# Kernel optimization log

Measured on AMD Instinct MI355X. Metric: run time of the kernel, lower is better.

## Reference

```python
import jax, jax.numpy as jnp
import numpy as np

D_MODEL = 2048
N_HEADS = 16
D_HEAD = 128
N_GROUPS = 4          # KV heads = N_HEADS // N_GROUPS = 4
D_FF = 2048           # hard-coded default in FeedForward
EPS = 1e-6


def setup_inputs() -> dict:
    key = jax.random.key(0)
    ks = jax.random.split(key, 16)
    B, S = 4, 1024
    Hkv = N_HEADS // N_GROUPS
    s = 0.02
    inp = {
        "x": jax.random.normal(ks[0], (B, S, D_MODEL), jnp.float32),
        "scale1": jnp.ones((D_MODEL,), jnp.float32),
        "Wq": jax.random.normal(ks[1], (D_MODEL, N_HEADS * D_HEAD), jnp.float32) * s,
        "bq": jnp.zeros((N_HEADS * D_HEAD,), jnp.float32),
        "Wk": jax.random.normal(ks[2], (D_MODEL, Hkv * D_HEAD), jnp.float32) * s,
        "bk": jnp.zeros((Hkv * D_HEAD,), jnp.float32),
        "Wv": jax.random.normal(ks[3], (D_MODEL, Hkv * D_HEAD), jnp.float32) * s,
        "bv": jnp.zeros((Hkv * D_HEAD,), jnp.float32),
        "Wo": jax.random.normal(ks[4], (N_HEADS * D_HEAD, D_MODEL), jnp.float32) * s,
        "bo": jnp.zeros((D_MODEL,), jnp.float32),
        "W1": jax.random.normal(ks[5], (D_MODEL, D_FF), jnp.float32) * s,
        "b1": jnp.zeros((D_FF,), jnp.float32),
        "W2": jax.random.normal(ks[6], (D_FF, D_MODEL), jnp.float32) * s,
        "b2": jnp.zeros((D_MODEL,), jnp.float32),
    }
    return inp


def _rmsnorm(x, scale):
    rms = jnp.sqrt(jnp.mean(x * x, axis=-1, keepdims=True) + EPS)
    return scale * (x / rms)


def reference(x, scale1, Wq, bq, Wk, bk, Wv, bv, Wo, bo, W1, b1, W2, b2):
    B, S, _ = x.shape
    Hkv = N_HEADS // N_GROUPS
    xn = _rmsnorm(x, scale1)  # [B,S,D]

    # GQA attention (prefill, step=None -> no cache)
    Q = (xn @ Wq + bq).reshape(B, S, N_HEADS, D_HEAD).transpose(0, 2, 1, 3)  # [B,H,S,d]
    K = (xn @ Wk + bk).reshape(B, S, Hkv, D_HEAD).transpose(0, 2, 1, 3)      # [B,Hkv,S,d]
    V = (xn @ Wv + bv).reshape(B, S, Hkv, D_HEAD).transpose(0, 2, 1, 3)
    Kr = jnp.repeat(K, N_GROUPS, axis=1)  # [B,H,S,d]
    Vr = jnp.repeat(V, N_GROUPS, axis=1)
    scores = jnp.einsum("bhqd,bhkd->bhqk", Q, Kr) / jnp.sqrt(jnp.float32(D_HEAD))
    attn = jax.nn.softmax(scores, axis=-1)
    out = jnp.einsum("bhqk,bhkd->bhqd", attn, Vr)  # [B,H,S,d]
    out = out.transpose(0, 2, 1, 3).reshape(B, S, N_HEADS * D_HEAD)
    x = x + out @ Wo + bo

    # Source bug preserved: FFN consumes rms_norm1 output, rms_norm2 is dead code
    h = xn @ W1 + b1
    h = h * jax.nn.sigmoid(h) * h  # x_ff * silu(x_ff)
    x = x + h @ W2 + b2
    return x
```

## Files before the change

### kernel.cpp

```cpp
#include <hip/hip_runtime.h>
#include <hip/hip_bf16.h>
#include <cstdint>

using bf16 = __hip_bfloat16;
typedef __attribute__((ext_vector_type(8))) __bf16 bf16x8;
typedef __attribute__((ext_vector_type(4))) float f32x4;

#define MFMA16(a, b, c) __builtin_amdgcn_mfma_f32_16x16x32_bf16((a), (b), (c), 0, 0, 0)

#if __has_builtin(__builtin_amdgcn_exp2f)
__device__ __forceinline__ float fexp2(float x) { return __builtin_amdgcn_exp2f(x); }
#else
__device__ __forceinline__ float fexp2(float x) { return exp2f(x); }
#endif

__device__ __forceinline__ void async16(void* lds_ptr, const void* gptr) {
  auto g = reinterpret_cast<__attribute__((address_space(1))) unsigned int*>(
      reinterpret_cast<uintptr_t>(gptr));
  auto l = reinterpret_cast<__attribute__((address_space(3))) unsigned int*>(
      static_cast<unsigned int>(reinterpret_cast<uintptr_t>(lds_ptr)));
  __builtin_amdgcn_global_load_lds(g, l, 16, 0, 0);
}

__global__ __launch_bounds__(256) void rmsnorm_cast_k(
    const float* __restrict__ x, const float* __restrict__ sc, bf16* __restrict__ xn) {
  const int row = blockIdx.x, tid = threadIdx.x;
  const float4* xr = (const float4*)(x + (size_t)row * 2048);
  float4 a = xr[tid * 2], b = xr[tid * 2 + 1];
  float ss = a.x * a.x + a.y * a.y + a.z * a.z + a.w * a.w +
             b.x * b.x + b.y * b.y + b.z * b.z + b.w * b.w;
#pragma unroll
  for (int d = 1; d < 64; d <<= 1) ss += __shfl_xor(ss, d);
  __shared__ float sm[4];
  if ((tid & 63) == 0) sm[tid >> 6] = ss;
  __syncthreads();
  const float rinv = rsqrtf((sm[0] + sm[1] + sm[2] + sm[3]) * (1.0f / 2048.0f) + 1e-6f);
  const float4* sp = (const float4*)sc;
  float4 s0 = sp[tid * 2], s1 = sp[tid * 2 + 1];
  union { bf16 h[8]; bf16x8 v; } o;
  o.h[0] = __float2bfloat16(a.x * rinv * s0.x);
  o.h[1] = __float2bfloat16(a.y * rinv * s0.y);
  o.h[2] = __float2bfloat16(a.z * rinv * s0.z);
  o.h[3] = __float2bfloat16(a.w * rinv * s0.w);
  o.h[4] = __float2bfloat16(b.x * rinv * s1.x);
  o.h[5] = __float2bfloat16(b.y * rinv * s1.y);
  o.h[6] = __float2bfloat16(b.z * rinv * s1.z);
  o.h[7] = __float2bfloat16(b.w * rinv * s1.w);
  *(bf16x8*)(xn + (size_t)row * 2048 + tid * 8) = o.v;
}

__global__ void transpose_cast_k(const float* __restrict__ W, bf16* __restrict__ Wt,
                                 int N, int ldt, int row_off, int k_off) {
  __shared__ float t[32][33];
  const int n0 = blockIdx.x * 32, k0 = blockIdx.y * 32;
  const int tx = threadIdx.x, ty = threadIdx.y;
#pragma unroll
  for (int i = 0; i < 4; ++i)
    t[ty + 8 * i][tx] = W[(size_t)(k0 + ty + 8 * i) * N + n0 + tx];
  __syncthreads();
#pragma unroll
  for (int i = 0; i < 4; ++i)
    Wt[(size_t)(row_off + n0 + ty + 8 * i) * ldt + k_off + k0 + tx] =
        __float2bfloat16(t[tx][ty + 8 * i]);
}

__global__ void transpose_v_k(const bf16* __restrict__ qkv, bf16* __restrict__ vtb) {
  __shared__ bf16 t[32][33];
  const int bh = blockIdx.z, b = bh >> 2, g = bh & 3;
  const int s0 = blockIdx.x * 32, d0 = blockIdx.y * 32;
  const int tx = threadIdx.x, ty = threadIdx.y;
#pragma unroll
  for (int i = 0; i < 4; ++i)
    t[ty + 8 * i][tx] =
        qkv[(size_t)(b * 1024 + s0 + ty + 8 * i) * 3072 + 2560 + g * 128 + d0 + tx];
  __syncthreads();
#pragma unroll
  for (int i = 0; i < 4; ++i)
    vtb[((size_t)bh * 128 + d0 + ty + 8 * i) * 1024 + s0 + tx] = t[tx][ty + 8 * i];
}

__global__ void concat_bias_k(const float* __restrict__ bq, const float* __restrict__ bk,
                              const float* __restrict__ bv, const float* __restrict__ b1,
                              const float* __restrict__ bo, const float* __restrict__ b2,
                              float* __restrict__ o) {
  const int i = blockIdx.x * 256 + threadIdx.x;
  if (i < 2048) o[i] = bq[i];
  else if (i < 2560) o[i] = bk[i - 2048];
  else if (i < 3072) o[i] = bv[i - 2560];
  else if (i < 5120) o[i] = b1[i - 3072];
  else o[i] = bo[i - 5120] + b2[i - 5120];
}

#define BARRIER() \
  { asm volatile("" ::: "memory"); __builtin_amdgcn_s_barrier(); asm volatile("" ::: "memory"); }
#define LGKM0() \
  { asm volatile("s_waitcnt lgkmcnt(0)" ::: "memory"); __builtin_amdgcn_sched_barrier(0); }
#define VM_MAIN                                                          \
  { if constexpr (LPS == 4) { asm volatile("s_waitcnt vmcnt(8)" ::: "memory"); } \
    else { asm volatile("s_waitcnt vmcnt(6)" ::: "memory"); }            \
    __builtin_amdgcn_sched_barrier(0); }
#define VM_ONE                                                           \
  { if constexpr (LPS == 4) { asm volatile("s_waitcnt vmcnt(4)" ::: "memory"); } \
    else { asm volatile("s_waitcnt vmcnt(3)" ::: "memory"); }            \
    __builtin_amdgcn_sched_barrier(0); }
#define VM_ZERO \
  { asm volatile("s_waitcnt vmcnt(0)" ::: "memory"); __builtin_amdgcn_sched_barrier(0); }

#define READ_AF(MILO)                                                              \
  { unsigned char* ab_ = lds + (h_ & 3) * SLOTA;                                   \
    _Pragma("unroll") for (int i_ = 0; i_ < MI / 2; ++i_) {                        \
      const int R_ = arow0 + ((MILO) + i_) * 16;                                   \
      af[i_] = *(const bf16x8*)(ab_ + R_ * 64 + ((hi ^ ((R_ >> 1) & 3)) << 4)); } }

#define READ_BF()                                                                  \
  { unsigned char* bb_ = lds + 4 * SLOTA + (h_ & 3) * SLOTB;                       \
    _Pragma("unroll") for (int j_ = 0; j_ < NJ; ++j_) {                            \
      const int S_ = bcol0 + j_ * 16;                                              \
      bf[j_] = *(const bf16x8*)(bb_ + S_ * 64 + ((hi ^ ((S_ >> 1) & 3)) << 4)); } }

#define MFMA_HALF(MILO)                                                            \
  __builtin_amdgcn_s_setprio(1);                                                   \
  _Pragma("unroll") for (int i_ = 0; i_ < MI / 2; ++i_)                            \
    _Pragma("unroll") for (int j_ = 0; j_ < NJ; ++j_)                              \
      acc[(MILO) + i_][j_] = MFMA16(af[i_], bf[j_], acc[(MILO) + i_][j_]);         \
  __builtin_amdgcn_s_setprio(0);

#define GSLOT(H, DOSTG, VMSTMT)                                                    \
  { const int h_ = (H);                                                            \
    READ_AF(0); READ_BF();                                                         \
    if (DOSTG) stgA(h_ + 3);                                                       \
    BARRIER(); LGKM0();                                                            \
    MFMA_HALF(0);                                                                  \
    BARRIER();                                                                     \
    READ_AF(MI / 2);                                                               \
    if (DOSTG) stgB(h_ + 3);                                                       \
    VMSTMT;                                                                        \
    BARRIER(); LGKM0();                                                            \
    MFMA_HALF(MI / 2);                                                             \
    BARRIER(); }

template <int MI, int NJ, int WM, int WN, int EPI>
__global__ __launch_bounds__(512, 1) void gemm8(
    const bf16* __restrict__ A, const bf16* __restrict__ A2,
    const bf16* __restrict__ Bt, const float* __restrict__ bias,
    const float* __restrict__ res, void* __restrict__ out0,
    void* __restrict__ out1, int K) {
  constexpr int BM = WM * MI * 16;
  constexpr int BN = WN * NJ * 16;
  constexpr int SLOTA = BM * 64;
  constexpr int SLOTB = BN * 64;
  constexpr int NSWA = SLOTA / 8192;
  constexpr int NSWB = SLOTB / 8192;
  constexpr int FRACB = SLOTB % 8192;
  constexpr int LPS = NSWA + NSWB;
  extern __shared__ unsigned char lds[];

  const int tid = threadIdx.x, lane = tid & 63, w = tid >> 6;
  const int wr = w / WN, wc = w % WN;
  const int hi = lane >> 4, lo = lane & 15;

  const int lid = blockIdx.y * 16 + blockIdx.x;
  const int xj = lid & 7, jj = lid >> 3;
  const int brow = ((xj & 3) * 4 + (jj & 3)) * BM;
  const int bcol = ((xj >> 2) * 8 + (jj >> 2)) * BN;

  const int NS = K >> 5;

  size_t offA[NSWA];
#pragma unroll
  for (int i = 0; i < NSWA; ++i) {
    const int o = i * 8192 + tid * 16;
    const int r = o >> 6;
    const int c = ((((o >> 4) & 3) ^ ((r >> 1) & 3)) << 3);
    offA[i] = (size_t)(brow + r) * 2048 + c;
  }
  const bf16* srcB[NSWB + (FRACB ? 1 : 0)];
#pragma unroll
  for (int i = 0; i < NSWB + (FRACB ? 1 : 0); ++i) {
    const int o = i * 8192 + tid * 16;
    const int r = o >> 6;
    const int c = ((((o >> 4) & 3) ^ ((r >> 1) & 3)) << 3);
    srcB[i] = Bt + (size_t)(bcol + r) * K + c;
  }

  auto stgA = [&](int h) {
    unsigned char* ab = lds + (h & 3) * SLOTA;
    const int kb = h * 32;
    const bf16* base;
    int ko;
    if constexpr (EPI == 1) { base = (kb < 2048) ? A : A2; ko = kb & 2047; }
    else { base = A; ko = kb; }
#pragma unroll
    for (int i = 0; i < NSWA; ++i)
      async16(ab + i * 8192 + tid * 16, base + offA[i] + ko);
  };
  auto stgB = [&](int h) {
    unsigned char* bb = lds + 4 * SLOTA + (h & 3) * SLOTB;
    const int kb = h * 32;
#pragma unroll
    for (int i = 0; i < NSWB; ++i)
      async16(bb + i * 8192 + tid * 16, srcB[i] + kb);
    if constexpr (FRACB != 0) {
      if (tid < FRACB / 16)
        async16(bb + NSWB * 8192 + tid * 16, srcB[NSWB] + kb);
    }
  };

  const int arow0 = wr * (MI * 16) + lo;
  const int bcol0 = wc * (NJ * 16) + lo;

  stgA(0); stgB(0); stgA(1); stgB(1); stgA(2); stgB(2);
  VM_MAIN;
  BARRIER();

  f32x4 acc[MI][NJ] = {};
  bf16x8 af[MI / 2], bf[NJ];

  for (int h = 0; h < NS - 3; ++h) { GSLOT(h, true, VM_MAIN); }
  GSLOT(NS - 3, false, VM_ONE);
  GSLOT(NS - 2, false, VM_ZERO);
  GSLOT(NS - 1, false, (void)0);

#pragma unroll
  for (int mi = 0; mi < MI; ++mi) {
    const int row = brow + wr * (MI * 16) + mi * 16 + hi * 4;
#pragma unroll
    for (int nj = 0; nj < NJ; ++nj) {
      const int col = bcol + wc * (NJ * 16) + nj * 16 + lo;
      const float bs = bias[col];
#pragma unroll
      for (int r = 0; r < 4; ++r) {
        float v = acc[mi][nj][r] + bs;
        if constexpr (EPI == 0) {
          if (col < 3072) {
            ((bf16*)out0)[(size_t)(row + r) * 3072 + col] = __float2bfloat16(v);
          } else {
            const float sg = 1.0f / (1.0f + __expf(-v));
            ((bf16*)out1)[(size_t)(row + r) * 2048 + (col - 3072)] =
                __float2bfloat16(v * sg * v);
          }
        } else {
          v += res[(size_t)(row + r) * 2048 + col];
          ((float*)out0)[(size_t)(row + r) * 2048 + col] = v;
        }
      }
    }
  }
}

__global__ __launch_bounds__(256, 4) void attn_fwd(
    const bf16* __restrict__ qkv, const bf16* __restrict__ vtb, bf16* __restrict__ out) {
  __shared__ __align__(16) unsigned char alds[40960];
  unsigned char* Ks = alds;
  unsigned char* Vs = alds + 16384;
  unsigned char* Ps = alds + 32768;
  const int tid = threadIdx.x, lane = tid & 63, w = tid >> 6;
  const int hi = lane >> 4, lo = lane & 15;
  const int qt = blockIdx.x, bh = blockIdx.y;
  const int b = bh >> 4, h = bh & 15, g = h >> 2;
  const size_t tok0 = (size_t)b * 1024;
  const int q0 = qt * 64;

  bf16x8 qf[4];
  {
    const bf16* qp = qkv + (tok0 + q0 + w * 16 + lo) * 3072 + h * 128 + hi * 8;
#pragma unroll
    for (int kc = 0; kc < 4; ++kc) qf[kc] = *(const bf16x8*)(qp + kc * 32);
  }

  float m2 = -1e30f, lsum = 0.f;
  f32x4 oacc[8] = {};
  const float c2 = 0.08838834764831845f * 1.44269504088896f;

  const int o = tid * 16;
  const bf16* kbase = qkv + tok0 * 3072 + 2048 + g * 128;
  const bf16* vbase = vtb + (size_t)(b * 4 + g) * 128 * 1024;
  unsigned char* Pw = Ps + w * 2048;

  for (int t = 0; t < 16; ++t) {
    const int kb = t * 64;
#pragma unroll
    for (int rd = 0; rd < 4; ++rd) {
      const int oo = o + rd * 4096;
      const int rK = oo >> 8, cK = ((oo >> 4) & 15) ^ (rK & 15);
      const int rV = oo >> 7, cV = ((oo >> 4) & 7) ^ (rV & 7);
      async16(Ks + oo, kbase + (size_t)(kb + rK) * 3072 + cK * 8);
      async16(Vs + oo, vbase + (size_t)rV * 1024 + kb + cV * 8);
    }
    __syncthreads();

    f32x4 sc[4] = {};
#pragma unroll
    for (int kc = 0; kc < 4; ++kc) {
#pragma unroll
      for (int kg = 0; kg < 4; ++kg) {
        const int row = kg * 16 + lo;
        bf16x8 kf = *(const bf16x8*)(Ks + row * 256 + ((((kc << 2) + hi) ^ (row & 15)) << 4));
        sc[kg] = MFMA16(kf, qf[kc], sc[kg]);
      }
    }

    float mx = sc[0][0];
#pragma unroll
    for (int kg = 0; kg < 4; ++kg)
#pragma unroll
      for (int r = 0; r < 4; ++r) mx = fmaxf(mx, sc[kg][r]);
    mx = fmaxf(mx, __shfl_xor(mx, 16));
    mx = fmaxf(mx, __shfl_xor(mx, 32));
    mx *= c2;
    const float mn = fmaxf(m2, mx);
    const float corr = fexp2(m2 - mn);
    m2 = mn;

    float rs = 0.f;
#pragma unroll
    for (int kg = 0; kg < 4; ++kg) {
      union { bf16 hh[4]; uint2 v; } pk;
#pragma unroll
      for (int r = 0; r < 4; ++r) {
        const float p = fexp2(sc[kg][r] * c2 - mn);
        rs += p;
        pk.hh[r] = __float2bfloat16(p);
      }
      *(uint2*)(Pw + lo * 128 + ((((kg << 1) + (hi >> 1)) ^ (lo & 7)) << 4) +
                ((hi & 1) << 3)) = pk.v;
    }
    rs += __shfl_xor(rs, 16);
    rs += __shfl_xor(rs, 32);
    lsum = lsum * corr + rs;

    float corr_r[4];
#pragma unroll
    for (int r = 0; r < 4; ++r) corr_r[r] = __shfl(corr, hi * 4 + r);
#pragma unroll
    for (int dg = 0; dg < 8; ++dg)
#pragma unroll
      for (int r = 0; r < 4; ++r) oacc[dg][r] *= corr_r[r];

    asm volatile("s_waitcnt lgkmcnt(0)" ::: "memory");

    bf16x8 pf[2];
#pragma unroll
    for (int kc = 0; kc < 2; ++kc)
      pf[kc] = *(const bf16x8*)(Pw + lo * 128 + ((((kc << 2) + hi) ^ (lo & 7)) << 4));
#pragma unroll
    for (int dg = 0; dg < 8; ++dg) {
#pragma unroll
      for (int kc = 0; kc < 2; ++kc) {
        const int vrow = dg * 16 + lo;
        bf16x8 vf = *(const bf16x8*)(Vs + vrow * 128 + ((((kc << 2) + hi) ^ (vrow & 7)) << 4));
        oacc[dg] = MFMA16(pf[kc], vf, oacc[dg]);
      }
    }
    __syncthreads();
  }

  const float linv = 1.0f / lsum;
  float lr[4];
#pragma unroll
  for (int r = 0; r < 4; ++r) lr[r] = __shfl(linv, hi * 4 + r);
  bf16* op = out + (tok0 + q0 + w * 16 + hi * 4) * 2048 + h * 128 + lo;
#pragma unroll
  for (int dg = 0; dg < 8; ++dg)
#pragma unroll
    for (int r = 0; r < 4; ++r)
      op[(size_t)r * 2048 + dg * 16] = __float2bfloat16(oacc[dg][r] * lr[r]);
}

extern "C" void kernel_launch(void* const* d_in, const int* in_sizes, int n_in,
                              void* d_out, int out_size, void* d_ws, size_t ws_size,
                              hipStream_t stream) {
  (void)in_sizes; (void)n_in; (void)out_size; (void)ws_size;
  const float* x  = (const float*)d_in[0];
  const float* s1 = (const float*)d_in[1];
  const float* Wq = (const float*)d_in[2];
  const float* bq = (const float*)d_in[3];
  const float* Wk = (const float*)d_in[4];
  const float* bk = (const float*)d_in[5];
  const float* Wv = (const float*)d_in[6];
  const float* bv = (const float*)d_in[7];
  const float* Wo = (const float*)d_in[8];
  const float* bo = (const float*)d_in[9];
  const float* W1 = (const float*)d_in[10];
  const float* b1 = (const float*)d_in[11];
  const float* W2 = (const float*)d_in[12];
  const float* b2 = (const float*)d_in[13];
  float* outp = (float*)d_out;

  char* ws = (char*)d_ws;
  bf16*  xn     = (bf16*)(ws + 0);
  bf16*  vtb    = (bf16*)(ws + 0);
  bf16*  wcatT  = (bf16*)(ws + 16777216);
  bf16*  attnb  = (bf16*)(ws + 16777216);
  float* bcat   = (float*)(ws + 37748736);
  bf16*  wcat2T = (bf16*)(ws + 37781504);
  bf16*  qkvb   = (bf16*)(ws + 54558720);
  bf16*  gbuf   = (bf16*)(ws + 79724544);

  const dim3 b32x8(32, 8);
  rmsnorm_cast_k<<<dim3(4096), dim3(256), 0, stream>>>(x, s1, xn);
  concat_bias_k<<<dim3(28), dim3(256), 0, stream>>>(bq, bk, bv, b1, bo, b2, bcat);
  transpose_cast_k<<<dim3(64, 64), b32x8, 0, stream>>>(Wq, wcatT, 2048, 2048, 0, 0);
  transpose_cast_k<<<dim3(16, 64), b32x8, 0, stream>>>(Wk, wcatT, 512, 2048, 2048, 0);
  transpose_cast_k<<<dim3(16, 64), b32x8, 0, stream>>>(Wv, wcatT, 512, 2048, 2560, 0);
  transpose_cast_k<<<dim3(64, 64), b32x8, 0, stream>>>(W1, wcatT, 2048, 2048, 3072, 0);
  transpose_cast_k<<<dim3(64, 64), b32x8, 0, stream>>>(Wo, wcat2T, 2048, 4096, 0, 0);
  transpose_cast_k<<<dim3(64, 64), b32x8, 0, stream>>>(W2, wcat2T, 2048, 4096, 0, 2048);
  gemm8<8, 5, 2, 4, 0><<<dim3(16, 16), dim3(512), 147456, stream>>>(
      xn, xn, wcatT, bcat, (const float*)nullptr, (void*)qkvb, (void*)gbuf, 2048);
  transpose_v_k<<<dim3(32, 4, 16), b32x8, 0, stream>>>(qkvb, vtb);
  attn_fwd<<<dim3(16, 64), dim3(256), 0, stream>>>(qkvb, vtb, attnb);
  gemm8<4, 4, 4, 2, 1><<<dim3(16, 16), dim3(512), 98304, stream>>>(
      attnb, gbuf, wcat2T, bcat + 5120, x, (void*)outp, (void*)nullptr, 4096);
}
```

Baseline: 254.2 us.

## Fuse prep kernels into one launch, add MFMA priority in attention, relax gemm bounds

Merges rmsnorm, bias concatenation and the six weight transpose-casts into a single prep kernel that dispatches on block index. This removes seven kernel launches and the gaps between them. The attention kernel now raises wave priority around its MFMA loops, and gemm8 launch bounds change from 1 to 2 blocks per SM, which can constrain register allocation. With 147KB of LDS per block, the second block per CU likely cannot be resident, so the bounds change may only tighten registers and cause spills.

```diff
diff --git a/kernel.cpp b/kernel.cpp
--- a/kernel.cpp
+++ b/kernel.cpp
@@ -22,38 +22,11 @@
   __builtin_amdgcn_global_load_lds(g, l, 16, 0, 0);
 }
 
-__global__ __launch_bounds__(256) void rmsnorm_cast_k(
-    const float* __restrict__ x, const float* __restrict__ sc, bf16* __restrict__ xn) {
-  const int row = blockIdx.x, tid = threadIdx.x;
-  const float4* xr = (const float4*)(x + (size_t)row * 2048);
-  float4 a = xr[tid * 2], b = xr[tid * 2 + 1];
-  float ss = a.x * a.x + a.y * a.y + a.z * a.z + a.w * a.w +
-             b.x * b.x + b.y * b.y + b.z * b.z + b.w * b.w;
-#pragma unroll
-  for (int d = 1; d < 64; d <<= 1) ss += __shfl_xor(ss, d);
-  __shared__ float sm[4];
-  if ((tid & 63) == 0) sm[tid >> 6] = ss;
-  __syncthreads();
-  const float rinv = rsqrtf((sm[0] + sm[1] + sm[2] + sm[3]) * (1.0f / 2048.0f) + 1e-6f);
-  const float4* sp = (const float4*)sc;
-  float4 s0 = sp[tid * 2], s1 = sp[tid * 2 + 1];
-  union { bf16 h[8]; bf16x8 v; } o;
-  o.h[0] = __float2bfloat16(a.x * rinv * s0.x);
-  o.h[1] = __float2bfloat16(a.y * rinv * s0.y);
-  o.h[2] = __float2bfloat16(a.z * rinv * s0.z);
-  o.h[3] = __float2bfloat16(a.w * rinv * s0.w);
-  o.h[4] = __float2bfloat16(b.x * rinv * s1.x);
-  o.h[5] = __float2bfloat16(b.y * rinv * s1.y);
-  o.h[6] = __float2bfloat16(b.z * rinv * s1.z);
-  o.h[7] = __float2bfloat16(b.w * rinv * s1.w);
-  *(bf16x8*)(xn + (size_t)row * 2048 + tid * 8) = o.v;
-}
-
-__global__ void transpose_cast_k(const float* __restrict__ W, bf16* __restrict__ Wt,
-                                 int N, int ldt, int row_off, int k_off) {
-  __shared__ float t[32][33];
-  const int n0 = blockIdx.x * 32, k0 = blockIdx.y * 32;
-  const int tx = threadIdx.x, ty = threadIdx.y;
+__device__ __forceinline__ void tr_body(const float* __restrict__ W,
+                                        bf16* __restrict__ Wt, int N, int ldt,
+                                        int row_off, int k_off, int lb, int nx,
+                                        float (*t)[33], int tx, int ty) {
+  const int n0 = (lb % nx) * 32, k0 = (lb / nx) * 32;
 #pragma unroll
   for (int i = 0; i < 4; ++i)
     t[ty + 8 * i][tx] = W[(size_t)(k0 + ty + 8 * i) * N + n0 + tx];
@@ -62,6 +35,66 @@
   for (int i = 0; i < 4; ++i)
     Wt[(size_t)(row_off + n0 + ty + 8 * i) * ldt + k_off + k0 + tx] =
         __float2bfloat16(t[tx][ty + 8 * i]);
+}
+
+__global__ __launch_bounds__(256) void prep_k(
+    const float* __restrict__ x, const float* __restrict__ s1, bf16* __restrict__ xn,
+    const float* __restrict__ Wq, const float* __restrict__ Wk,
+    const float* __restrict__ Wv, const float* __restrict__ W1,
+    const float* __restrict__ Wo, const float* __restrict__ W2,
+    bf16* __restrict__ wcatT, bf16* __restrict__ wcat2T,
+    const float* __restrict__ bq, const float* __restrict__ bk,
+    const float* __restrict__ bv, const float* __restrict__ b1,
+    const float* __restrict__ bo, const float* __restrict__ b2,
+    float* __restrict__ bcat) {
+  __shared__ float t[32][33];
+  const int tid = threadIdx.x;
+  int bid = blockIdx.x;
+  if (bid < 4096) {
+    const int row = bid;
+    const float4* xr = (const float4*)(x + (size_t)row * 2048);
+    float4 a = xr[tid * 2], b = xr[tid * 2 + 1];
+    float ss = a.x * a.x + a.y * a.y + a.z * a.z + a.w * a.w +
+               b.x * b.x + b.y * b.y + b.z * b.z + b.w * b.w;
+#pragma unroll
+    for (int d = 1; d < 64; d <<= 1) ss += __shfl_xor(ss, d);
+    if ((tid & 63) == 0) t[0][tid >> 6] = ss;
+    __syncthreads();
+    const float rinv =
+        rsqrtf((t[0][0] + t[0][1] + t[0][2] + t[0][3]) * (1.0f / 2048.0f) + 1e-6f);
+    const float4* sp = (const float4*)s1;
+    float4 s0 = sp[tid * 2], s1v = sp[tid * 2 + 1];
+    union { bf16 h[8]; bf16x8 v; } o;
+    o.h[0] = __float2bfloat16(a.x * rinv * s0.x);
+    o.h[1] = __float2bfloat16(a.y * rinv * s0.y);
+    o.h[2] = __float2bfloat16(a.z * rinv * s0.z);
+    o.h[3] = __float2bfloat16(a.w * rinv * s0.w);
+    o.h[4] = __float2bfloat16(b.x * rinv * s1v.x);
+    o.h[5] = __float2bfloat16(b.y * rinv * s1v.y);
+    o.h[6] = __float2bfloat16(b.z * rinv * s1v.z);
+    o.h[7] = __float2bfloat16(b.w * rinv * s1v.w);
+    *(bf16x8*)(xn + (size_t)row * 2048 + tid * 8) = o.v;
+    return;
+  }
+  if (bid < 4124) {
+    const int i = (bid - 4096) * 256 + tid;
+    float v;
+    if (i < 2048) v = bq[i];
+    else if (i < 2560) v = bk[i - 2048];
+    else if (i < 3072) v = bv[i - 2560];
+    else if (i < 5120) v = b1[i - 3072];
+    else v = bo[i - 5120] + b2[i - 5120];
+    bcat[i] = v;
+    return;
+  }
+  bid -= 4124;
+  const int tx = tid & 31, ty = tid >> 5;
+  if (bid < 4096)       tr_body(Wq, wcatT, 2048, 2048, 0, 0, bid, 64, t, tx, ty);
+  else if (bid < 5120)  tr_body(Wk, wcatT, 512, 2048, 2048, 0, bid - 4096, 16, t, tx, ty);
+  else if (bid < 6144)  tr_body(Wv, wcatT, 512, 2048, 2560, 0, bid - 5120, 16, t, tx, ty);
+  else if (bid < 10240) tr_body(W1, wcatT, 2048, 2048, 3072, 0, bid - 6144, 64, t, tx, ty);
+  else if (bid < 14336) tr_body(Wo, wcat2T, 2048, 4096, 0, 0, bid - 10240, 64, t, tx, ty);
+  else                  tr_body(W2, wcat2T, 2048, 4096, 0, 2048, bid - 14336, 64, t, tx, ty);
 }
 
 __global__ void transpose_v_k(const bf16* __restrict__ qkv, bf16* __restrict__ vtb) {
@@ -77,18 +110,6 @@
 #pragma unroll
   for (int i = 0; i < 4; ++i)
     vtb[((size_t)bh * 128 + d0 + ty + 8 * i) * 1024 + s0 + tx] = t[tx][ty + 8 * i];
-}
-
-__global__ void concat_bias_k(const float* __restrict__ bq, const float* __restrict__ bk,
-                              const float* __restrict__ bv, const float* __restrict__ b1,
-                              const float* __restrict__ bo, const float* __restrict__ b2,
-                              float* __restrict__ o) {
-  const int i = blockIdx.x * 256 + threadIdx.x;
-  if (i < 2048) o[i] = bq[i];
-  else if (i < 2560) o[i] = bk[i - 2048];
-  else if (i < 3072) o[i] = bv[i - 2560];
-  else if (i < 5120) o[i] = b1[i - 3072];
-  else o[i] = bo[i - 5120] + b2[i - 5120];
 }
 
 #define BARRIER() \
@@ -140,7 +161,7 @@
     BARRIER(); }
 
 template <int MI, int NJ, int WM, int WN, int EPI>
-__global__ __launch_bounds__(512, 1) void gemm8(
+__global__ __launch_bounds__(512, 2) void gemm8(
     const bf16* __restrict__ A, const bf16* __restrict__ A2,
     const bf16* __restrict__ Bt, const float* __restrict__ bias,
     const float* __restrict__ res, void* __restrict__ out0,
@@ -290,6 +311,7 @@
     __syncthreads();
 
     f32x4 sc[4] = {};
+    __builtin_amdgcn_s_setprio(1);
 #pragma unroll
     for (int kc = 0; kc < 4; ++kc) {
 #pragma unroll
@@ -299,6 +321,7 @@
         sc[kg] = MFMA16(kf, qf[kc], sc[kg]);
       }
     }
+    __builtin_amdgcn_s_setprio(0);
 
     float mx = sc[0][0];
 #pragma unroll
@@ -343,6 +366,7 @@
 #pragma unroll
     for (int kc = 0; kc < 2; ++kc)
       pf[kc] = *(const bf16x8*)(Pw + lo * 128 + ((((kc << 2) + hi) ^ (lo & 7)) << 4));
+    __builtin_amdgcn_s_setprio(1);
 #pragma unroll
     for (int dg = 0; dg < 8; ++dg) {
 #pragma unroll
@@ -352,6 +376,7 @@
         oacc[dg] = MFMA16(pf[kc], vf, oacc[dg]);
       }
     }
+    __builtin_amdgcn_s_setprio(0);
     __syncthreads();
   }
 
@@ -397,18 +422,12 @@
   bf16*  qkvb   = (bf16*)(ws + 54558720);
   bf16*  gbuf   = (bf16*)(ws + 79724544);
 
-  const dim3 b32x8(32, 8);
-  rmsnorm_cast_k<<<dim3(4096), dim3(256), 0, stream>>>(x, s1, xn);
-  concat_bias_k<<<dim3(28), dim3(256), 0, stream>>>(bq, bk, bv, b1, bo, b2, bcat);
-  transpose_cast_k<<<dim3(64, 64), b32x8, 0, stream>>>(Wq, wcatT, 2048, 2048, 0, 0);
-  transpose_cast_k<<<dim3(16, 64), b32x8, 0, stream>>>(Wk, wcatT, 512, 2048, 2048, 0);
-  transpose_cast_k<<<dim3(16, 64), b32x8, 0, stream>>>(Wv, wcatT, 512, 2048, 2560, 0);
-  transpose_cast_k<<<dim3(64, 64), b32x8, 0, stream>>>(W1, wcatT, 2048, 2048, 3072, 0);
-  transpose_cast_k<<<dim3(64, 64), b32x8, 0, stream>>>(Wo, wcat2T, 2048, 4096, 0, 0);
-  transpose_cast_k<<<dim3(64, 64), b32x8, 0, stream>>>(W2, wcat2T, 2048, 4096, 0, 2048);
+  prep_k<<<dim3(22556), dim3(256), 0, stream>>>(
+      x, s1, xn, Wq, Wk, Wv, W1, Wo, W2, wcatT, wcat2T,
+      bq, bk, bv, b1, bo, b2, bcat);
   gemm8<8, 5, 2, 4, 0><<<dim3(16, 16), dim3(512), 147456, stream>>>(
       xn, xn, wcatT, bcat, (const float*)nullptr, (void*)qkvb, (void*)gbuf, 2048);
-  transpose_v_k<<<dim3(32, 4, 16), b32x8, 0, stream>>>(qkvb, vtb);
+  transpose_v_k<<<dim3(32, 4, 16), dim3(32, 8), 0, stream>>>(qkvb, vtb);
   attn_fwd<<<dim3(16, 64), dim3(256), 0, stream>>>(qkvb, vtb, attnb);
   gemm8<4, 4, 4, 2, 1><<<dim3(16, 16), dim3(512), 98304, stream>>>(
       attnb, gbuf, wcat2T, bcat + 5120, x, (void*)outp, (void*)nullptr, 4096);
```

Measured after the change: 240.8 us. 5.3% less time.
